# Performance work log

Measured on AMD Instinct MI355X. Metric: run time of the kernel, lower is better.

## Reference

```python
import jax, jax.numpy as jnp
import numpy as np

D = 1024  # model_embedding_dim
T = 512   # n_future_dx
B = 16384


def setup_inputs() -> dict:
    key = jax.random.key(0)
    k1, k2, k3, k4, k5 = jax.random.split(key, 5)
    x = jax.random.normal(k1, (B, D), dtype=jnp.float32)
    # Linear layers: torch nn.Linear stores weight [out, in], bias [out]
    s = 1.0 / np.sqrt(D)
    Wh = jax.random.uniform(k2, (T, D), jnp.float32, -s, s)
    bh = jax.random.uniform(k3, (T,), jnp.float32, -s, s)
    Wb = jax.random.uniform(k4, (1, D), jnp.float32, -s, s)
    bb = jax.random.uniform(k5, (1,), jnp.float32, -s, s)
    return {"x": x, "Wh": Wh, "bh": bh, "Wb": Wb, "bb": bb}


def reference(x, Wh, bh, Wb, bb):
    # hazards = relu(x @ Wh^T + bh)  -> [B, T]
    hazards = jax.nn.relu(jnp.einsum('bd,td->bt', x, Wh) + bh)
    # masked expand-and-sum with upper-triangular mask (mask[i,j]=1 iff i<=j)
    # equals inclusive prefix sum along T.
    cum = jnp.cumsum(hazards, axis=1)
    base = jnp.einsum('bd,od->bo', x, Wb) + bb  # [B, 1]
    return cum + base
```

## Files before the change

### kernel.cpp

```cpp
#include <hip/hip_runtime.h>
#include <hip/hip_bf16.h>


typedef __bf16 bf16x8 __attribute__((ext_vector_type(8)));
typedef __bf16 bf16x4 __attribute__((ext_vector_type(4)));
typedef float f32x4 __attribute__((ext_vector_type(4)));

typedef const __attribute__((address_space(1))) void* gas_cptr;
typedef __attribute__((address_space(3))) void* las_ptr;

#define BM 64
#define BK 32
#define NKIT 32
#define TDIM 512
#define DDIM 1024

__global__ __launch_bounds__(256) void cvt_wh_kernel(const float* __restrict__ src,
                                                     __bf16* __restrict__ dst) {
    const int i = (blockIdx.x * 256 + threadIdx.x) * 4;
    const float4 v = *reinterpret_cast<const float4*>(src + i);
    bf16x4 o;
    o[0] = (__bf16)v.x; o[1] = (__bf16)v.y; o[2] = (__bf16)v.z; o[3] = (__bf16)v.w;
    *reinterpret_cast<bf16x4*>(dst + i) = o;
}

__device__ __forceinline__ int swz(int row) { return ((row >> 1) & 3) << 4; }

__global__ __launch_bounds__(512, 4) void survival_kernel(
    const float* __restrict__ x,
    const __bf16* __restrict__ Whb,
    const float* __restrict__ bh,
    const float* __restrict__ Wb,
    const float* __restrict__ bbp,
    float* __restrict__ out)
{
    __shared__ __align__(16) char Alds[2][BM * 64];
    __shared__ __align__(16) char Blds[2][TDIM * 64];
    __shared__ float baseLds[BM];
    __shared__ float totLds[BM][4];

    const int tid  = threadIdx.x;
    const int lane = tid & 63;
    const int wid  = tid >> 6;
    const int wm   = wid >> 2;
    const int wn   = wid & 3;
    const int brow = blockIdx.x * BM;

    const float bb0 = bbp[0];

    const int ar = tid >> 3;
    const int au = tid & 7;
    const float* xrow  = x  + (size_t)(brow + ar) * DDIM + au * 4;
    const float* wbrow = Wb + au * 4;
    char* const a_dst0 = &Alds[0][0] + ar * 64 + ((au * 8) ^ swz(ar));

    const int b_row0 = wid * 64 + (lane >> 2);
    const int b_slot = lane & 3;

    float bpart = 0.f;
    f32x4 acc[2][8];
#pragma unroll
    for (int rt = 0; rt < 2; ++rt)
#pragma unroll
        for (int n = 0; n < 8; ++n)
            acc[rt][n] = (f32x4){0.f, 0.f, 0.f, 0.f};

    auto stage = [&](int buf, int it) {
        const int k0 = it * BK;
#pragma unroll
        for (int c = 0; c < 4; ++c) {
            const int row  = b_row0 + c * 16;
            const int colb = (b_slot * 16) ^ swz(row);
            const __bf16* g = Whb + (size_t)row * DDIM + k0 + (colb >> 1);
            char* l = &Blds[buf][0] + (wid * 64 + c * 16) * 64;
            __builtin_amdgcn_global_load_lds((gas_cptr)(const void*)g,
                                             (las_ptr)(void*)l, 16, 0, 0);
        }
        const float4 xv = *reinterpret_cast<const float4*>(xrow + k0);
        const float4 wv = *reinterpret_cast<const float4*>(wbrow + k0);
        bpart += xv.x * wv.x + xv.y * wv.y + xv.z * wv.z + xv.w * wv.w;
        bf16x4 av;
        av[0] = (__bf16)xv.x; av[1] = (__bf16)xv.y; av[2] = (__bf16)xv.z; av[3] = (__bf16)xv.w;
        *reinterpret_cast<bf16x4*>(a_dst0 + buf * (BM * 64)) = av;
    };

    auto compute = [&](int buf) {
        const char* Ab = &Blds[0][0];
        (void)Ab;
        const char* Abuf = &Alds[buf][0];
        const char* Bbuf = &Blds[buf][0];
        const int slot = (lane >> 4) * 16;
        bf16x8 af[2];
#pragma unroll
        for (int rt = 0; rt < 2; ++rt) {
            const int row = wm * 32 + rt * 16 + (lane & 15);
            af[rt] = *reinterpret_cast<const bf16x8*>(Abuf + row * 64 + (slot ^ swz(row)));
        }
#pragma unroll
        for (int n = 0; n < 8; ++n) {
            const int trow = wn * 128 + n * 16 + (lane & 15);
            const bf16x8 bfr = *reinterpret_cast<const bf16x8*>(
                Bbuf + trow * 64 + (slot ^ swz(trow)));
            acc[0][n] = __builtin_amdgcn_mfma_f32_16x16x32_bf16(af[0], bfr, acc[0][n], 0, 0, 0);
            acc[1][n] = __builtin_amdgcn_mfma_f32_16x16x32_bf16(af[1], bfr, acc[1][n], 0, 0, 0);
        }
    };

    stage(0, 0);
    __syncthreads();
#pragma unroll 2
    for (int it = 0; it < NKIT; ++it) {
        const int cur = it & 1;
        if (it + 1 < NKIT) stage(cur ^ 1, it + 1);
        compute(cur);
        __syncthreads();
    }

    bpart += __shfl_xor(bpart, 1, 8);
    bpart += __shfl_xor(bpart, 2, 8);
    bpart += __shfl_xor(bpart, 4, 8);
    if ((tid & 7) == 0) baseLds[tid >> 3] = bpart + bb0;

    float bhv[8];
#pragma unroll
    for (int n = 0; n < 8; ++n)
        bhv[n] = bh[wn * 128 + n * 16 + (lane & 15)];

    float carry[2][4] = {{0.f, 0.f, 0.f, 0.f}, {0.f, 0.f, 0.f, 0.f}};
#pragma unroll
    for (int n = 0; n < 8; ++n) {
#pragma unroll
        for (int rt = 0; rt < 2; ++rt) {
#pragma unroll
            for (int j = 0; j < 4; ++j) {
                float v = fmaxf(acc[rt][n][j] + bhv[n], 0.f);
#pragma unroll
                for (int off = 1; off < 16; off <<= 1) {
                    const float u = __shfl_up(v, (unsigned)off, 16);
                    if ((lane & 15) >= off) v += u;
                }
                v += carry[rt][j];
                carry[rt][j] = __shfl(v, 15, 16);
                acc[rt][n][j] = v;
            }
        }
    }

    if ((lane & 15) == 0) {
#pragma unroll
        for (int rt = 0; rt < 2; ++rt)
#pragma unroll
            for (int j = 0; j < 4; ++j) {
                const int r = wm * 32 + rt * 16 + (lane >> 4) * 4 + j;
                totLds[r][wn] = carry[rt][j];
            }
    }
    __syncthreads();

#pragma unroll
    for (int rt = 0; rt < 2; ++rt) {
#pragma unroll
        for (int j = 0; j < 4; ++j) {
            const int r = wm * 32 + rt * 16 + (lane >> 4) * 4 + j;
            float rc = baseLds[r];
            if (wn > 0) rc += totLds[r][0];
            if (wn > 1) rc += totLds[r][1];
            if (wn > 2) rc += totLds[r][2];
            float* orow = out + (size_t)(brow + r) * TDIM + wn * 128 + (lane & 15);
#pragma unroll
            for (int n = 0; n < 8; ++n)
                orow[n * 16] = acc[rt][n][j] + rc;
        }
    }
}

extern "C" void kernel_launch(void* const* d_in, const int* in_sizes, int n_in,
                              void* d_out, int out_size, void* d_ws, size_t ws_size,
                              hipStream_t stream) {
    const float* x  = (const float*)d_in[0];
    const float* Wh = (const float*)d_in[1];
    const float* bh = (const float*)d_in[2];
    const float* Wb = (const float*)d_in[3];
    const float* bb = (const float*)d_in[4];
    float* out = (float*)d_out;
    __bf16* Whb = (__bf16*)d_ws;

    cvt_wh_kernel<<<512, 256, 0, stream>>>(Wh, Whb);
    survival_kernel<<<256, 512, 0, stream>>>(x, Whb, bh, Wb, bb, out);
}
```

Measured before the change: 156.0 us.

## Double K tile, use 16 waves per block, and split-phase prefetch with manual waitcnts

Raises the K tile from 32 to 64, which halves the number of main-loop iterations and barriers. Doubles the block to 1024 threads (16 waves), giving each wave a narrower 64-column slice of T. Splits staging into an issue phase and a write phase so the global loads for the next tile are in flight while the current tile computes, using explicit s_waitcnt and s_barrier in place of __syncthreads. The cost is twice the LDS per block (about 160KB), which probably limits residency to one block per CU, plus fine-grained waitcnt logic that may be fragile.

```diff
diff --git a/kernel.cpp b/kernel.cpp
--- a/kernel.cpp
+++ b/kernel.cpp
@@ -10,10 +10,17 @@
 typedef __attribute__((address_space(3))) void* las_ptr;
 
 #define BM 64
-#define BK 32
-#define NKIT 32
+#define BK 64
+#define NKIT 16
 #define TDIM 512
 #define DDIM 1024
+#define ASZ (BM * 128)
+#define BSZ (TDIM * 128)
+
+#define WAIT_TOP()  asm volatile("s_waitcnt vmcnt(6) lgkmcnt(0)" ::: "memory")
+#define WAIT_LGKM() asm volatile("s_waitcnt lgkmcnt(0)" ::: "memory")
+#define WAIT_VM0()  asm volatile("s_waitcnt vmcnt(0)" ::: "memory")
+#define SBAR()      __builtin_amdgcn_s_barrier()
 
 __global__ __launch_bounds__(256) void cvt_wh_kernel(const float* __restrict__ src,
                                                      __bf16* __restrict__ dst) {
@@ -24,9 +31,9 @@
     *reinterpret_cast<bf16x4*>(dst + i) = o;
 }
 
-__device__ __forceinline__ int swz(int row) { return ((row >> 1) & 3) << 4; }
-
-__global__ __launch_bounds__(512, 4) void survival_kernel(
+__device__ __forceinline__ int swz(int row) { return ((row >> 1) & 7) << 4; }
+
+__global__ __launch_bounds__(1024, 4) void survival_kernel(
     const float* __restrict__ x,
     const __bf16* __restrict__ Whb,
     const float* __restrict__ bh,
@@ -34,101 +41,116 @@
     const float* __restrict__ bbp,
     float* __restrict__ out)
 {
-    __shared__ __align__(16) char Alds[2][BM * 64];
-    __shared__ __align__(16) char Blds[2][TDIM * 64];
+    __shared__ __align__(16) char Alds[2][ASZ];
+    __shared__ __align__(16) char Blds[2][BSZ];
     __shared__ float baseLds[BM];
-    __shared__ float totLds[BM][4];
+    __shared__ float totLds[BM][8];
 
     const int tid  = threadIdx.x;
     const int lane = tid & 63;
     const int wid  = tid >> 6;
-    const int wm   = wid >> 2;
-    const int wn   = wid & 3;
+    const int wm   = wid >> 3;
+    const int wn   = wid & 7;
     const int brow = blockIdx.x * BM;
 
     const float bb0 = bbp[0];
 
-    const int ar = tid >> 3;
-    const int au = tid & 7;
-    const float* xrow  = x  + (size_t)(brow + ar) * DDIM + au * 4;
-    const float* wbrow = Wb + au * 4;
-    char* const a_dst0 = &Alds[0][0] + ar * 64 + ((au * 8) ^ swz(ar));
-
-    const int b_row0 = wid * 64 + (lane >> 2);
-    const int b_slot = lane & 3;
+    const int ar = tid >> 4;
+    const int ac = tid & 15;
+    const float* xrow  = x  + (size_t)(brow + ar) * DDIM + ac * 4;
+    const float* wbrow = Wb + ac * 4;
+    char* const a_dst0 = &Alds[0][0] + ar * 128 + ((ac * 8) ^ swz(ar));
+
+    const int b_row0 = wid * 32 + (lane >> 3);
+    const int b_slot = lane & 7;
 
     float bpart = 0.f;
-    f32x4 acc[2][8];
+    f32x4 acc[2][4];
 #pragma unroll
     for (int rt = 0; rt < 2; ++rt)
 #pragma unroll
-        for (int n = 0; n < 8; ++n)
+        for (int n = 0; n < 4; ++n)
             acc[rt][n] = (f32x4){0.f, 0.f, 0.f, 0.f};
 
-    auto stage = [&](int buf, int it) {
+    float4 xv, wv;
+
+    auto stage_issue = [&](int buf, int it) {
         const int k0 = it * BK;
+        xv = *reinterpret_cast<const float4*>(xrow + k0);
+        wv = *reinterpret_cast<const float4*>(wbrow + k0);
 #pragma unroll
         for (int c = 0; c < 4; ++c) {
-            const int row  = b_row0 + c * 16;
+            const int row  = b_row0 + c * 8;
             const int colb = (b_slot * 16) ^ swz(row);
             const __bf16* g = Whb + (size_t)row * DDIM + k0 + (colb >> 1);
-            char* l = &Blds[buf][0] + (wid * 64 + c * 16) * 64;
+            char* l = &Blds[0][0] + buf * BSZ + (wid * 32 + c * 8) * 128;
             __builtin_amdgcn_global_load_lds((gas_cptr)(const void*)g,
                                              (las_ptr)(void*)l, 16, 0, 0);
         }
-        const float4 xv = *reinterpret_cast<const float4*>(xrow + k0);
-        const float4 wv = *reinterpret_cast<const float4*>(wbrow + k0);
+    };
+
+    auto stage_write = [&](int buf) {
         bpart += xv.x * wv.x + xv.y * wv.y + xv.z * wv.z + xv.w * wv.w;
         bf16x4 av;
-        av[0] = (__bf16)xv.x; av[1] = (__bf16)xv.y; av[2] = (__bf16)xv.z; av[3] = (__bf16)xv.w;
-        *reinterpret_cast<bf16x4*>(a_dst0 + buf * (BM * 64)) = av;
+        av[0] = (__bf16)xv.x; av[1] = (__bf16)xv.y;
+        av[2] = (__bf16)xv.z; av[3] = (__bf16)xv.w;
+        *reinterpret_cast<bf16x4*>(a_dst0 + buf * ASZ) = av;
     };
 
     auto compute = [&](int buf) {
-        const char* Ab = &Blds[0][0];
-        (void)Ab;
-        const char* Abuf = &Alds[buf][0];
-        const char* Bbuf = &Blds[buf][0];
-        const int slot = (lane >> 4) * 16;
-        bf16x8 af[2];
-#pragma unroll
-        for (int rt = 0; rt < 2; ++rt) {
-            const int row = wm * 32 + rt * 16 + (lane & 15);
-            af[rt] = *reinterpret_cast<const bf16x8*>(Abuf + row * 64 + (slot ^ swz(row)));
-        }
-#pragma unroll
-        for (int n = 0; n < 8; ++n) {
-            const int trow = wn * 128 + n * 16 + (lane & 15);
-            const bf16x8 bfr = *reinterpret_cast<const bf16x8*>(
-                Bbuf + trow * 64 + (slot ^ swz(trow)));
-            acc[0][n] = __builtin_amdgcn_mfma_f32_16x16x32_bf16(af[0], bfr, acc[0][n], 0, 0, 0);
-            acc[1][n] = __builtin_amdgcn_mfma_f32_16x16x32_bf16(af[1], bfr, acc[1][n], 0, 0, 0);
+        const char* Ab = &Alds[0][0] + buf * ASZ;
+        const char* Bb = &Blds[0][0] + buf * BSZ;
+#pragma unroll
+        for (int h = 0; h < 2; ++h) {
+            const int slot = (h * 4 + (lane >> 4)) * 16;
+            bf16x8 af[2];
+#pragma unroll
+            for (int rt = 0; rt < 2; ++rt) {
+                const int row = wm * 32 + rt * 16 + (lane & 15);
+                af[rt] = *reinterpret_cast<const bf16x8*>(Ab + row * 128 + (slot ^ swz(row)));
+            }
+#pragma unroll
+            for (int n = 0; n < 4; ++n) {
+                const int trow = wn * 64 + n * 16 + (lane & 15);
+                const bf16x8 bfr = *reinterpret_cast<const bf16x8*>(
+                    Bb + trow * 128 + (slot ^ swz(trow)));
+                acc[0][n] = __builtin_amdgcn_mfma_f32_16x16x32_bf16(af[0], bfr, acc[0][n], 0, 0, 0);
+                acc[1][n] = __builtin_amdgcn_mfma_f32_16x16x32_bf16(af[1], bfr, acc[1][n], 0, 0, 0);
+            }
         }
     };
 
-    stage(0, 0);
-    __syncthreads();
-#pragma unroll 2
-    for (int it = 0; it < NKIT; ++it) {
+    stage_issue(0, 0);
+    stage_write(0);
+    for (int it = 0; it < NKIT - 1; ++it) {
         const int cur = it & 1;
-        if (it + 1 < NKIT) stage(cur ^ 1, it + 1);
+        const int nxt = cur ^ 1;
+        stage_issue(nxt, it + 1);
+        WAIT_TOP();
+        SBAR();
         compute(cur);
-        __syncthreads();
-    }
-
-    bpart += __shfl_xor(bpart, 1, 8);
-    bpart += __shfl_xor(bpart, 2, 8);
-    bpart += __shfl_xor(bpart, 4, 8);
-    if ((tid & 7) == 0) baseLds[tid >> 3] = bpart + bb0;
-
-    float bhv[8];
-#pragma unroll
-    for (int n = 0; n < 8; ++n)
-        bhv[n] = bh[wn * 128 + n * 16 + (lane & 15)];
-
-    float carry[2][4] = {{0.f, 0.f, 0.f, 0.f}, {0.f, 0.f, 0.f, 0.f}};
-#pragma unroll
-    for (int n = 0; n < 8; ++n) {
+        stage_write(nxt);
+        WAIT_LGKM();
+        SBAR();
+    }
+    WAIT_VM0();
+    SBAR();
+    compute((NKIT - 1) & 1);
+
+    bpart += __shfl_xor(bpart, 1, 16);
+    bpart += __shfl_xor(bpart, 2, 16);
+    bpart += __shfl_xor(bpart, 4, 16);
+    bpart += __shfl_xor(bpart, 8, 16);
+    if ((tid & 15) == 0) baseLds[tid >> 4] = bpart + bb0;
+
+    float bhv[4];
+#pragma unroll
+    for (int n = 0; n < 4; ++n)
+        bhv[n] = bh[wn * 64 + n * 16 + (lane & 15)];
+
+    float carry[2][4] = {{0.f,0.f,0.f,0.f},{0.f,0.f,0.f,0.f}};
+#pragma unroll
+    for (int n = 0; n < 4; ++n) {
 #pragma unroll
         for (int rt = 0; rt < 2; ++rt) {
 #pragma unroll
@@ -163,12 +185,12 @@
         for (int j = 0; j < 4; ++j) {
             const int r = wm * 32 + rt * 16 + (lane >> 4) * 4 + j;
             float rc = baseLds[r];
-            if (wn > 0) rc += totLds[r][0];
-            if (wn > 1) rc += totLds[r][1];
-            if (wn > 2) rc += totLds[r][2];
-            float* orow = out + (size_t)(brow + r) * TDIM + wn * 128 + (lane & 15);
-#pragma unroll
-            for (int n = 0; n < 8; ++n)
+#pragma unroll
+            for (int w = 0; w < 7; ++w)
+                if (w < wn) rc += totLds[r][w];
+            float* orow = out + (size_t)(brow + r) * TDIM + wn * 64 + (lane & 15);
+#pragma unroll
+            for (int n = 0; n < 4; ++n)
                 orow[n * 16] = acc[rt][n][j] + rc;
         }
     }
@@ -186,5 +208,5 @@
     __bf16* Whb = (__bf16*)d_ws;
 
     cvt_wh_kernel<<<512, 256, 0, stream>>>(Wh, Whb);
-    survival_kernel<<<256, 512, 0, stream>>>(x, Whb, bh, Wb, bb, out);
+    survival_kernel<<<256, 1024, 0, stream>>>(x, Whb, bh, Wb, bb, out);
 }
```

Result: faster. 134.6 us (-13.7%).

## Triple-buffer LDS with register-staged x loads and 1x8 warp tiling

Applied to the files above, without the earlier changes.

Replaces the double-buffered loop with a three-stage pipeline. Loads for tile t+2 are issued while tile t computes, x values are staged in registers and written to LDS after compute, and explicit vmcnt waits plus raw barriers replace __syncthreads. The warp layout changes from 2x4 to 1x8 over T, so each warp covers all 64 rows and 64 columns, reusing B fragments across 4 row tiles. The cross-warp prefix combine is adjusted for 8 column groups. This raises LDS use and lowers the occupancy hint to 2, trading occupancy for deeper latency hiding.

```diff
diff --git a/kernel.cpp b/kernel.cpp
--- a/kernel.cpp
+++ b/kernel.cpp
@@ -14,6 +14,14 @@
 #define NKIT 32
 #define TDIM 512
 #define DDIM 1024
+#define ASZ (BM * 64)
+#define BSZ (TDIM * 64)
+
+#define WAITV12()  asm volatile("s_waitcnt vmcnt(12) lgkmcnt(0)" ::: "memory")
+#define WAITV6()   asm volatile("s_waitcnt vmcnt(6) lgkmcnt(0)"  ::: "memory")
+#define WAITV0()   asm volatile("s_waitcnt vmcnt(0) lgkmcnt(0)"  ::: "memory")
+#define WAIT_LGKM() asm volatile("s_waitcnt lgkmcnt(0)" ::: "memory")
+#define SBAR()     __builtin_amdgcn_s_barrier()
 
 __global__ __launch_bounds__(256) void cvt_wh_kernel(const float* __restrict__ src,
                                                      __bf16* __restrict__ dst) {
@@ -24,9 +32,9 @@
     *reinterpret_cast<bf16x4*>(dst + i) = o;
 }
 
-__device__ __forceinline__ int swz(int row) { return ((row >> 1) & 3) << 4; }
-
-__global__ __launch_bounds__(512, 4) void survival_kernel(
+__device__ __forceinline__ int swz64(int row) { return ((row >> 1) & 3) << 4; }
+
+__global__ __launch_bounds__(512, 2) void survival_kernel(
     const float* __restrict__ x,
     const __bf16* __restrict__ Whb,
     const float* __restrict__ bh,
@@ -34,103 +42,121 @@
     const float* __restrict__ bbp,
     float* __restrict__ out)
 {
-    __shared__ __align__(16) char Alds[2][BM * 64];
-    __shared__ __align__(16) char Blds[2][TDIM * 64];
+    __shared__ __align__(16) char Alds[3][ASZ];
+    __shared__ __align__(16) char Blds[3][BSZ];
     __shared__ float baseLds[BM];
-    __shared__ float totLds[BM][4];
+    __shared__ float totLds[BM][8];
 
     const int tid  = threadIdx.x;
     const int lane = tid & 63;
     const int wid  = tid >> 6;
-    const int wm   = wid >> 2;
-    const int wn   = wid & 3;
     const int brow = blockIdx.x * BM;
-
     const float bb0 = bbp[0];
 
     const int ar = tid >> 3;
-    const int au = tid & 7;
-    const float* xrow  = x  + (size_t)(brow + ar) * DDIM + au * 4;
-    const float* wbrow = Wb + au * 4;
-    char* const a_dst0 = &Alds[0][0] + ar * 64 + ((au * 8) ^ swz(ar));
-
-    const int b_row0 = wid * 64 + (lane >> 2);
-    const int b_slot = lane & 3;
+    const int ac = tid & 7;
+    const float* xrow = x + (size_t)(brow + ar) * DDIM + ac * 4;
+    const float* wbp  = Wb + ac * 4;
+    const int a_off = ar * 64 + (((ac >> 1) * 16) ^ swz64(ar)) + (ac & 1) * 8;
+
+    const int b_rbase = wid * 64 + (lane >> 2);
+    const int b_slot  = lane & 3;
 
     float bpart = 0.f;
-    f32x4 acc[2][8];
-#pragma unroll
-    for (int rt = 0; rt < 2; ++rt)
-#pragma unroll
-        for (int n = 0; n < 8; ++n)
+    f32x4 acc[4][4];
+#pragma unroll
+    for (int rt = 0; rt < 4; ++rt)
+#pragma unroll
+        for (int n = 0; n < 4; ++n)
             acc[rt][n] = (f32x4){0.f, 0.f, 0.f, 0.f};
 
-    auto stage = [&](int buf, int it) {
+    float4 xr0, wr0, xr1, wr1;
+
+    auto issueT = [&](int buf, int it, int slot) {
         const int k0 = it * BK;
+        if (slot == 0) { xr0 = *reinterpret_cast<const float4*>(xrow + k0);
+                         wr0 = *reinterpret_cast<const float4*>(wbp + k0); }
+        else           { xr1 = *reinterpret_cast<const float4*>(xrow + k0);
+                         wr1 = *reinterpret_cast<const float4*>(wbp + k0); }
 #pragma unroll
         for (int c = 0; c < 4; ++c) {
-            const int row  = b_row0 + c * 16;
-            const int colb = (b_slot * 16) ^ swz(row);
+            const int row  = b_rbase + c * 16;
+            const int colb = (b_slot * 16) ^ swz64(row);
             const __bf16* g = Whb + (size_t)row * DDIM + k0 + (colb >> 1);
             char* l = &Blds[buf][0] + (wid * 64 + c * 16) * 64;
             __builtin_amdgcn_global_load_lds((gas_cptr)(const void*)g,
                                              (las_ptr)(void*)l, 16, 0, 0);
         }
-        const float4 xv = *reinterpret_cast<const float4*>(xrow + k0);
-        const float4 wv = *reinterpret_cast<const float4*>(wbrow + k0);
+    };
+
+    auto writeT = [&](int buf, int slot) {
+        const float4 xv = slot ? xr1 : xr0;
+        const float4 wv = slot ? wr1 : wr0;
         bpart += xv.x * wv.x + xv.y * wv.y + xv.z * wv.z + xv.w * wv.w;
         bf16x4 av;
-        av[0] = (__bf16)xv.x; av[1] = (__bf16)xv.y; av[2] = (__bf16)xv.z; av[3] = (__bf16)xv.w;
-        *reinterpret_cast<bf16x4*>(a_dst0 + buf * (BM * 64)) = av;
+        av[0] = (__bf16)xv.x; av[1] = (__bf16)xv.y;
+        av[2] = (__bf16)xv.z; av[3] = (__bf16)xv.w;
+        *reinterpret_cast<bf16x4*>(&Alds[buf][0] + a_off) = av;
     };
 
     auto compute = [&](int buf) {
-        const char* Ab = &Blds[0][0];
-        (void)Ab;
-        const char* Abuf = &Alds[buf][0];
-        const char* Bbuf = &Blds[buf][0];
-        const int slot = (lane >> 4) * 16;
-        bf16x8 af[2];
-#pragma unroll
-        for (int rt = 0; rt < 2; ++rt) {
-            const int row = wm * 32 + rt * 16 + (lane & 15);
-            af[rt] = *reinterpret_cast<const bf16x8*>(Abuf + row * 64 + (slot ^ swz(row)));
-        }
-#pragma unroll
-        for (int n = 0; n < 8; ++n) {
-            const int trow = wn * 128 + n * 16 + (lane & 15);
+        const char* Ab = &Alds[buf][0];
+        const char* Bb = &Blds[buf][0];
+        const int qslot = (lane >> 4) * 16;
+        bf16x8 af[4];
+#pragma unroll
+        for (int rt = 0; rt < 4; ++rt) {
+            const int row = rt * 16 + (lane & 15);
+            af[rt] = *reinterpret_cast<const bf16x8*>(Ab + row * 64 + (qslot ^ swz64(row)));
+        }
+#pragma unroll
+        for (int n = 0; n < 4; ++n) {
+            const int trow = wid * 64 + n * 16 + (lane & 15);
             const bf16x8 bfr = *reinterpret_cast<const bf16x8*>(
-                Bbuf + trow * 64 + (slot ^ swz(trow)));
-            acc[0][n] = __builtin_amdgcn_mfma_f32_16x16x32_bf16(af[0], bfr, acc[0][n], 0, 0, 0);
-            acc[1][n] = __builtin_amdgcn_mfma_f32_16x16x32_bf16(af[1], bfr, acc[1][n], 0, 0, 0);
+                Bb + trow * 64 + (qslot ^ swz64(trow)));
+#pragma unroll
+            for (int rt = 0; rt < 4; ++rt)
+                acc[rt][n] = __builtin_amdgcn_mfma_f32_16x16x32_bf16(af[rt], bfr, acc[rt][n], 0, 0, 0);
         }
     };
 
-    stage(0, 0);
-    __syncthreads();
-#pragma unroll 2
-    for (int it = 0; it < NKIT; ++it) {
-        const int cur = it & 1;
-        if (it + 1 < NKIT) stage(cur ^ 1, it + 1);
-        compute(cur);
-        __syncthreads();
+    issueT(0, 0, 0);
+    issueT(1, 1, 1);
+    writeT(0, 0);
+
+#pragma unroll
+    for (int t = 0; t < NKIT; ++t) {
+        if (t + 2 < NKIT) issueT((t + 2) % 3, t + 2, t & 1);
+        if (t + 2 < NKIT)      WAITV12();
+        else if (t + 1 < NKIT) WAITV6();
+        else                   WAITV0();
+        SBAR();
+        compute(t % 3);
+        if (t + 1 < NKIT) writeT((t + 1) % 3, (t + 1) & 1);
+        WAIT_LGKM();
+        SBAR();
     }
 
     bpart += __shfl_xor(bpart, 1, 8);
     bpart += __shfl_xor(bpart, 2, 8);
     bpart += __shfl_xor(bpart, 4, 8);
-    if ((tid & 7) == 0) baseLds[tid >> 3] = bpart + bb0;
-
-    float bhv[8];
-#pragma unroll
-    for (int n = 0; n < 8; ++n)
-        bhv[n] = bh[wn * 128 + n * 16 + (lane & 15)];
-
-    float carry[2][4] = {{0.f, 0.f, 0.f, 0.f}, {0.f, 0.f, 0.f, 0.f}};
-#pragma unroll
-    for (int n = 0; n < 8; ++n) {
-#pragma unroll
-        for (int rt = 0; rt < 2; ++rt) {
+    if (ac == 0) baseLds[ar] = bpart + bb0;
+
+    float bhv[4];
+#pragma unroll
+    for (int n = 0; n < 4; ++n)
+        bhv[n] = bh[wid * 64 + n * 16 + (lane & 15)];
+
+    float carry[4][4];
+#pragma unroll
+    for (int rt = 0; rt < 4; ++rt)
+#pragma unroll
+        for (int j = 0; j < 4; ++j) carry[rt][j] = 0.f;
+
+#pragma unroll
+    for (int n = 0; n < 4; ++n) {
+#pragma unroll
+        for (int rt = 0; rt < 4; ++rt) {
 #pragma unroll
             for (int j = 0; j < 4; ++j) {
                 float v = fmaxf(acc[rt][n][j] + bhv[n], 0.f);
@@ -148,27 +174,27 @@
 
     if ((lane & 15) == 0) {
 #pragma unroll
-        for (int rt = 0; rt < 2; ++rt)
+        for (int rt = 0; rt < 4; ++rt)
 #pragma unroll
             for (int j = 0; j < 4; ++j) {
-                const int r = wm * 32 + rt * 16 + (lane >> 4) * 4 + j;
-                totLds[r][wn] = carry[rt][j];
+                const int r = rt * 16 + (lane >> 4) * 4 + j;
+                totLds[r][wid] = carry[rt][j];
             }
     }
     __syncthreads();
 
 #pragma unroll
-    for (int rt = 0; rt < 2; ++rt) {
+    for (int rt = 0; rt < 4; ++rt) {
 #pragma unroll
         for (int j = 0; j < 4; ++j) {
-            const int r = wm * 32 + rt * 16 + (lane >> 4) * 4 + j;
+            const int r = rt * 16 + (lane >> 4) * 4 + j;
             float rc = baseLds[r];
-            if (wn > 0) rc += totLds[r][0];
-            if (wn > 1) rc += totLds[r][1];
-            if (wn > 2) rc += totLds[r][2];
-            float* orow = out + (size_t)(brow + r) * TDIM + wn * 128 + (lane & 15);
-#pragma unroll
-            for (int n = 0; n < 8; ++n)
+#pragma unroll
+            for (int w = 0; w < 7; ++w)
+                if (w < wid) rc += totLds[r][w];
+            float* orow = out + (size_t)(brow + r) * TDIM + wid * 64 + (lane & 15);
+#pragma unroll
+            for (int n = 0; n < 4; ++n)
                 orow[n * 16] = acc[rt][n][j] + rc;
         }
     }
```

New measurement: 151.4 us. 1.03x faster.
